# Optimization experiments

Measured on AMD Instinct MI355X. Metric: run time of the kernel, lower is better.

## Reference

```python
import jax, jax.numpy as jnp
import numpy as np

DIM = 512
HEADS = 16
WIN = 8  # window size (square)
B, H, W = 8, 128, 128
N = WIN * WIN  # tokens per window


def _relative_position_index(wh, ww):
    coords = np.stack(np.meshgrid(np.arange(wh), np.arange(ww), indexing='ij'))  # [2,wh,ww]
    cf = coords.reshape(2, -1)
    rel = cf[:, :, None] - cf[:, None, :]  # [2,n,n]
    rel = rel.transpose(1, 2, 0).astype(np.int32)
    rel[:, :, 0] += wh - 1
    rel[:, :, 1] += ww - 1
    rel[:, :, 0] *= 2 * ww - 1
    return rel.sum(-1)  # [n,n]


def setup_inputs() -> dict:
    key = jax.random.key(0)
    ks = jax.random.split(key, 8)
    std = 0.02
    return {
        'xa': jax.random.normal(ks[0], (B, DIM, H, W), jnp.float32),
        'xb': jax.random.normal(ks[1], (B, DIM, H, W), jnp.float32),
        'Wq': jax.random.normal(ks[2], (DIM, DIM), jnp.float32) * std,
        'bq': jnp.zeros((DIM,), jnp.float32),
        'Wkv': jax.random.normal(ks[3], (2 * DIM, DIM), jnp.float32) * std,
        'bkv': jnp.zeros((2 * DIM,), jnp.float32),
        'Wo': jax.random.normal(ks[4], (DIM, DIM), jnp.float32) * std,
        'bo': jnp.zeros((DIM,), jnp.float32),
        'rpb_table': jax.random.normal(ks[5], ((2 * WIN - 1) ** 2, HEADS), jnp.float32) * 0.01,
        'rel_idx': jnp.asarray(_relative_position_index(WIN, WIN)),
    }


def _windows(x):
    # [B,C,H,W] -> [B*r1*r2, N, C]
    b, c, h, w = x.shape
    r1, r2 = h // WIN, w // WIN
    x = x.reshape(b, c, r1, WIN, r2, WIN).transpose(0, 2, 4, 3, 5, 1)
    return x.reshape(b * r1 * r2, N, c)


def reference(xa, xb, Wq, bq, Wkv, bkv, Wo, bo, rpb_table, rel_idx):
    b, c, h, w = xa.shape
    r1, r2 = h // WIN, w // WIN
    head_dim = c // HEADS
    scale = head_dim ** -0.5

    qa = _windows(xa)  # [BM, N, C]
    kb = _windows(xb)

    q = jnp.einsum('bnc,oc->bno', qa, Wq) + bq
    kv = jnp.einsum('bnc,oc->bno', kb, Wkv) + bkv
    k, v = jnp.split(kv, 2, axis=2)
    q = q * scale

    def heads(t):  # [BM,N,C] -> [BM,H,N,hd]
        return t.reshape(t.shape[0], N, HEADS, head_dim).transpose(0, 2, 1, 3)

    q, k, v = heads(q), heads(k), heads(v)

    attn = jnp.einsum('bhmc,bhnc->bhmn', q, k)
    bias = rpb_table[rel_idx.reshape(-1)].reshape(N, N, HEADS).transpose(2, 0, 1)
    attn = attn + bias[None]
    attn = jax.nn.softmax(attn, axis=-1)

    out = jnp.einsum('bhmn,bhnc->bhmc', attn, v)
    out = out.transpose(0, 2, 1, 3).reshape(-1, N, c)
    out = jnp.einsum('bnc,oc->bno', out, Wo) + bo

    # [B*r1*r2, N, C] -> [B, C, H, W]
    out = out.reshape(b, r1, r2, WIN, WIN, c).transpose(0, 5, 1, 3, 2, 4)
    return out.reshape(b, c, h, w)
```

## Files before the change

kernel.cpp:

```cpp
#include <hip/hip_runtime.h>
#include <hip/hip_bf16.h>
#include <cstdint>
#include <cstddef>

typedef __attribute__((ext_vector_type(4))) float f32x4;
typedef __attribute__((ext_vector_type(8))) __bf16 bf16x8;
typedef __attribute__((ext_vector_type(8))) unsigned short ushort8;

__device__ __forceinline__ unsigned short f2b(float f) {
  unsigned int u = __float_as_uint(f);
  u = (u + 0x7fffu + ((u >> 16) & 1u)) >> 16;
  return (unsigned short)u;
}
__device__ __forceinline__ float b2f(unsigned short u) {
  return __uint_as_float(((unsigned int)u) << 16);
}

__device__ __forceinline__ f32x4 mfma_bf16(bf16x8 a, bf16x8 b, f32x4 c) {
  return __builtin_amdgcn_mfma_f32_16x16x32_bf16(a, b, c, 0, 0, 0);
}


__global__ void cvtw(const float* __restrict__ s, unsigned short* __restrict__ d, int n) {
  int i = blockIdx.x * 256 + threadIdx.x;
  if (i < n) d[i] = f2b(s[i]);
}

__global__ void bias_pre(const float* __restrict__ rpb, const int* __restrict__ rel,
                         float* __restrict__ biasf) {
  int i = blockIdx.x * 256 + threadIdx.x;
  int h = i >> 12, mn = i & 4095;
  biasf[i] = rpb[rel[mn] * 16 + h];
}

__global__ __launch_bounds__(256) void win_tr(const float* __restrict__ src,
                                              unsigned short* __restrict__ dst) {
  __shared__ float T[64 * 65];
  int bx = blockIdx.x;
  int win = bx >> 3, cg = bx & 7;
  int b = win >> 8, r1 = (win >> 4) & 15, r2 = win & 15;
  int h0 = r1 * 8, w0c = r2 * 8, c0 = cg * 64;
  int t = threadIdx.x;
#pragma unroll
  for (int pp = 0; pp < 2; ++pp) {
    int p = t + pp * 256;
    int cl = p >> 3, dy = p & 7;
    const float* sp = src + (((size_t)(b * 512 + c0 + cl) * 128 + (h0 + dy)) * 128 + w0c);
    float4 v0 = *(const float4*)sp;
    float4 v1 = *(const float4*)(sp + 4);
    int rb = dy * 8;
    T[(rb + 0) * 65 + cl] = v0.x; T[(rb + 1) * 65 + cl] = v0.y;
    T[(rb + 2) * 65 + cl] = v0.z; T[(rb + 3) * 65 + cl] = v0.w;
    T[(rb + 4) * 65 + cl] = v1.x; T[(rb + 5) * 65 + cl] = v1.y;
    T[(rb + 6) * 65 + cl] = v1.z; T[(rb + 7) * 65 + cl] = v1.w;
  }
  __syncthreads();
  int n = t >> 2, q = t & 3;
  union { unsigned short u[8]; int4 v; } pk0, pk1;
#pragma unroll
  for (int i = 0; i < 8; ++i) pk0.u[i] = f2b(T[n * 65 + q * 16 + i]);
#pragma unroll
  for (int i = 0; i < 8; ++i) pk1.u[i] = f2b(T[n * 65 + q * 16 + 8 + i]);
  size_t o = ((size_t)win * 64 + n) * 512 + c0 + q * 16;
  *(int4*)(dst + o) = pk0.v;
  *(int4*)(dst + o + 8) = pk1.v;
}

__global__ __launch_bounds__(256) void inv_tr(const unsigned short* __restrict__ Ot,
                                              float* __restrict__ out) {
  __shared__ float T[64 * 65];
  int bx = blockIdx.x;
  int win = bx >> 3, cg = bx & 7;
  int b = win >> 8, r1 = (win >> 4) & 15, r2 = win & 15;
  int h0 = r1 * 8, w0c = r2 * 8, c0 = cg * 64;
  int t = threadIdx.x;
  int n = t >> 2, q = t & 3;
  const unsigned short* sp = Ot + ((size_t)win * 64 + n) * 512 + c0 + q * 16;
  union { unsigned short u[8]; int4 v; } r0, r1u;
  r0.v = *(const int4*)sp;
  r1u.v = *(const int4*)(sp + 8);
#pragma unroll
  for (int i = 0; i < 8; ++i) {
    T[(q * 16 + i) * 65 + n] = b2f(r0.u[i]);
    T[(q * 16 + 8 + i) * 65 + n] = b2f(r1u.u[i]);
  }
  __syncthreads();
#pragma unroll
  for (int pp = 0; pp < 2; ++pp) {
    int p = t + pp * 256;
    int cl = p >> 3, dy = p & 7;
    int rb = dy * 8;
    float4 a, bv;
    a.x = T[cl * 65 + rb + 0]; a.y = T[cl * 65 + rb + 1];
    a.z = T[cl * 65 + rb + 2]; a.w = T[cl * 65 + rb + 3];
    bv.x = T[cl * 65 + rb + 4]; bv.y = T[cl * 65 + rb + 5];
    bv.z = T[cl * 65 + rb + 6]; bv.w = T[cl * 65 + rb + 7];
    float* dp = out + (((size_t)(b * 512 + c0 + cl) * 128 + (h0 + dy)) * 128 + w0c);
    *(float4*)dp = a;
    *(float4*)(dp + 4) = bv;
  }
}

template <int MODE, int NTL>
__global__ __launch_bounds__(256) void gemm_nt(const unsigned short* __restrict__ A,
                                               const unsigned short* __restrict__ W,
                                               const float* __restrict__ bias,
                                               unsigned short* __restrict__ out0,
                                               unsigned short* __restrict__ out1) {
  __shared__ __align__(16) unsigned short As[2][128 * 40];
  __shared__ __align__(16) unsigned short Bs[2][128 * 40];
  int bid = blockIdx.x;
  int cpx = gridDim.x >> 3;
  int wg = (bid & 7) * cpx + (bid >> 3);
  int tn = wg & ((1 << NTL) - 1);
  int tm = wg >> NTL;
  int m0 = tm * 128, n0 = tn * 128;
  int tid = threadIdx.x;
  int w = tid >> 6, lane = tid & 63, g = lane >> 4, c16 = lane & 15;
  int wr = w >> 1, wc = w & 1;
  int srow = tid >> 2, sq = tid & 3;
  const unsigned short* Ap0 = A + (size_t)(m0 + srow) * 512 + sq * 8;
  const unsigned short* Ap1 = Ap0 + 64 * 512;
  const unsigned short* Wp0 = W + (size_t)(n0 + srow) * 512 + sq * 8;
  const unsigned short* Wp1 = Wp0 + 64 * 512;
  int sA0 = srow * 40 + sq * 8;
  int sA1 = (srow + 64) * 40 + sq * 8;
  int aoff = (wr * 64 + c16) * 40 + g * 8;
  int boff = (wc * 64 + c16) * 40 + g * 8;

  int4 ra0 = *(const int4*)Ap0;
  int4 ra1 = *(const int4*)Ap1;
  int4 rb0 = *(const int4*)Wp0;
  int4 rb1 = *(const int4*)Wp1;
  *(int4*)&As[0][sA0] = ra0; *(int4*)&As[0][sA1] = ra1;
  *(int4*)&Bs[0][sA0] = rb0; *(int4*)&Bs[0][sA1] = rb1;
  __syncthreads();

  f32x4 z = {0.f, 0.f, 0.f, 0.f};
  f32x4 acc[4][4];
#pragma unroll
  for (int i = 0; i < 4; ++i)
#pragma unroll
    for (int j = 0; j < 4; ++j) acc[i][j] = z;

  for (int kt = 0; kt < 16; ++kt) {
    int cur = kt & 1;
    bf16x8 af[4], bfv[4];
#pragma unroll
    for (int i = 0; i < 4; ++i) {
      af[i]  = *(const bf16x8*)&As[cur][aoff + i * 640];
      bfv[i] = *(const bf16x8*)&Bs[cur][boff + i * 640];
    }
    if (kt < 15) {
      ra0 = *(const int4*)(Ap0 + (kt + 1) * 32);
      ra1 = *(const int4*)(Ap1 + (kt + 1) * 32);
      rb0 = *(const int4*)(Wp0 + (kt + 1) * 32);
      rb1 = *(const int4*)(Wp1 + (kt + 1) * 32);
    }
#pragma unroll
    for (int fm = 0; fm < 4; ++fm)
#pragma unroll
      for (int fn = 0; fn < 4; ++fn)
        acc[fm][fn] = mfma_bf16(af[fm], bfv[fn], acc[fm][fn]);
    if (kt < 15) {
      int nxt = cur ^ 1;
      *(int4*)&As[nxt][sA0] = ra0; *(int4*)&As[nxt][sA1] = ra1;
      *(int4*)&Bs[nxt][sA0] = rb0; *(int4*)&Bs[nxt][sA1] = rb1;
    }
    __syncthreads();
  }

  int mbase = m0 + wr * 64;
  int nbase = n0 + wc * 64;
#pragma unroll
  for (int fn = 0; fn < 4; ++fn) {
    int o = nbase + fn * 16 + c16;
    float bv = bias[o];
#pragma unroll
    for (int fm = 0; fm < 4; ++fm) {
      f32x4 v = acc[fm][fn];
#pragma unroll
      for (int r = 0; r < 4; ++r) {
        int tt = mbase + fm * 16 + g * 4 + r;
        float val = v[r] + bv;
        if constexpr (MODE == 0) {
          val *= 0.17677669529663688f;
          size_t idx = ((size_t)(tt >> 6) * 16 + (o >> 5)) * 2048 + (size_t)(tt & 63) * 32 + (o & 31);
          out0[idx] = f2b(val);
        } else if constexpr (MODE == 1) {
          int ol = o & 511;
          unsigned short* dst = (o < 512) ? out0 : out1;
          size_t idx = ((size_t)(tt >> 6) * 16 + (ol >> 5)) * 2048 + (size_t)(tt & 63) * 32 + (ol & 31);
          dst[idx] = f2b(val);
        } else {
          out0[(size_t)tt * 512 + o] = f2b(val);
        }
      }
    }
  }
}

#define SWZ(row, byte) ((byte) ^ (((((row) & 7) ^ (((row) >> 3) & 1))) << 4))

__global__ __launch_bounds__(256) void attn_win(const unsigned short* __restrict__ Qb,
                                                const unsigned short* __restrict__ Kb,
                                                const unsigned short* __restrict__ Vb,
                                                const float* __restrict__ biasf,
                                                unsigned short* __restrict__ Oattn) {
  __shared__ __align__(16) unsigned short Pl[4][4096];
  __shared__ __align__(16) unsigned short Vt[4][2048];
  int win = blockIdx.x;
  int tid = threadIdx.x, w = tid >> 6, lane = tid & 63;
  int g = lane >> 4, c16 = lane & 15;
  char* P  = (char*)Pl[w];
  char* VT = (char*)Vt[w];
  f32x4 z = {0.f, 0.f, 0.f, 0.f};
  for (int hh = 0; hh < 4; ++hh) {
    int h = w * 4 + hh;
    const bf16x8* qp = (const bf16x8*)(Qb + ((size_t)win * 16 + h) * 2048);
    const bf16x8* kp = (const bf16x8*)(Kb + ((size_t)win * 16 + h) * 2048);
    bf16x8 qf[4], kf[4];
#pragma unroll
    for (int i = 0; i < 4; ++i) {
      qf[i] = qp[(i * 16 + c16) * 4 + g];
      kf[i] = kp[(i * 16 + c16) * 4 + g];
    }
    f32x4 s[4][4];
#pragma unroll
    for (int i = 0; i < 4; ++i)
#pragma unroll
      for (int j = 0; j < 4; ++j) s[i][j] = z;
#pragma unroll
    for (int fm = 0; fm < 4; ++fm)
#pragma unroll
      for (int fn = 0; fn < 4; ++fn)
        s[fm][fn] = mfma_bf16(qf[fm], kf[fn], s[fm][fn]);

    const float* bh = biasf + h * 4096;
#pragma unroll
    for (int fm = 0; fm < 4; ++fm) {
#pragma unroll
      for (int r = 0; r < 4; ++r) {
        int m = fm * 16 + g * 4 + r;
        float vals[4];
#pragma unroll
        for (int fn = 0; fn < 4; ++fn)
          vals[fn] = s[fm][fn][r] + bh[m * 64 + fn * 16 + c16];
        float mx = fmaxf(fmaxf(vals[0], vals[1]), fmaxf(vals[2], vals[3]));
        mx = fmaxf(mx, __shfl_xor(mx, 1));
        mx = fmaxf(mx, __shfl_xor(mx, 2));
        mx = fmaxf(mx, __shfl_xor(mx, 4));
        mx = fmaxf(mx, __shfl_xor(mx, 8));
        float sum = 0.f;
#pragma unroll
        for (int fn = 0; fn < 4; ++fn) { vals[fn] = __expf(vals[fn] - mx); sum += vals[fn]; }
        sum += __shfl_xor(sum, 1);
        sum += __shfl_xor(sum, 2);
        sum += __shfl_xor(sum, 4);
        sum += __shfl_xor(sum, 8);
        float inv = 1.0f / sum;
#pragma unroll
        for (int fn = 0; fn < 4; ++fn) {
          int col = fn * 16 + c16;
          int byte = SWZ(m, m * 128 + col * 2);
          *(unsigned short*)(P + byte) = f2b(vals[fn] * inv);
        }
      }
    }
    const ushort8* vp = (const ushort8*)(Vb + ((size_t)win * 16 + h) * 2048);
#pragma unroll
    for (int i = 0; i < 4; ++i) {
      ushort8 vv = vp[(i * 16 + c16) * 4 + g];
#pragma unroll
      for (int j = 0; j < 8; ++j) {
        int row = g * 8 + j;
        int col = i * 16 + c16;
        int byte = SWZ(row, row * 128 + col * 2);
        *(unsigned short*)(VT + byte) = vv[j];
      }
    }
    f32x4 oa[4][2];
#pragma unroll
    for (int i = 0; i < 4; ++i) { oa[i][0] = z; oa[i][1] = z; }
#pragma unroll
    for (int ks = 0; ks < 2; ++ks) {
      bf16x8 pa[4], vbf[2];
#pragma unroll
      for (int fm = 0; fm < 4; ++fm) {
        int row = fm * 16 + c16;
        pa[fm] = *(const bf16x8*)(P + SWZ(row, row * 128 + ks * 64 + g * 16));
      }
#pragma unroll
      for (int fc = 0; fc < 2; ++fc) {
        int row = fc * 16 + c16;
        vbf[fc] = *(const bf16x8*)(VT + SWZ(row, row * 128 + ks * 64 + g * 16));
      }
#pragma unroll
      for (int fm = 0; fm < 4; ++fm)
#pragma unroll
        for (int fc = 0; fc < 2; ++fc)
          oa[fm][fc] = mfma_bf16(pa[fm], vbf[fc], oa[fm][fc]);
    }
#pragma unroll
    for (int fm = 0; fm < 4; ++fm)
#pragma unroll
      for (int fc = 0; fc < 2; ++fc)
#pragma unroll
        for (int r = 0; r < 4; ++r) {
          int m = fm * 16 + g * 4 + r;
          Oattn[((size_t)win * 64 + m) * 512 + h * 32 + fc * 16 + c16] = f2b(oa[fm][fc][r]);
        }
  }
}

extern "C" void kernel_launch(void* const* d_in, const int* in_sizes, int n_in,
                              void* d_out, int out_size, void* d_ws, size_t ws_size,
                              hipStream_t stream) {
  const float* xa  = (const float*)d_in[0];
  const float* xb  = (const float*)d_in[1];
  const float* Wq  = (const float*)d_in[2];
  const float* bq  = (const float*)d_in[3];
  const float* Wkv = (const float*)d_in[4];
  const float* bkv = (const float*)d_in[5];
  const float* Wo  = (const float*)d_in[6];
  const float* bo  = (const float*)d_in[7];
  const float* rpb = (const float*)d_in[8];
  const int*   rel = (const int*)d_in[9];
  float* out = (float*)d_out;

  char* ws = (char*)d_ws;
  unsigned short* R0 = (unsigned short*)ws;
  unsigned short* Qb = (unsigned short*)(ws + (size_t)134217728);
  unsigned short* Ot = Qb;
  unsigned short* Kb = (unsigned short*)d_out;
  unsigned short* Vb = Kb + (size_t)67108864;
  char* extra        = ws + (size_t)268435456;
  float* biasf          = (float*)extra;
  unsigned short* WqB   = (unsigned short*)(extra + 262144);
  unsigned short* WkvB  = (unsigned short*)(extra + 262144 + 524288);
  unsigned short* WoB   = (unsigned short*)(extra + 262144 + 524288 + 1048576);

  cvtw<<<1024, 256, 0, stream>>>(Wq,  WqB,  262144);
  cvtw<<<2048, 256, 0, stream>>>(Wkv, WkvB, 524288);
  cvtw<<<1024, 256, 0, stream>>>(Wo,  WoB,  262144);
  bias_pre<<<256, 256, 0, stream>>>(rpb, rel, biasf);

  win_tr<<<16384, 256, 0, stream>>>(xa, R0);
  gemm_nt<0, 2><<<4096, 256, 0, stream>>>(R0, WqB, bq, Qb, nullptr);
  win_tr<<<16384, 256, 0, stream>>>(xb, R0);
  gemm_nt<1, 3><<<8192, 256, 0, stream>>>(R0, WkvB, bkv, Kb, Vb);
  attn_win<<<2048, 256, 0, stream>>>(Qb, Kb, Vb, biasf, R0);
  gemm_nt<2, 2><<<4096, 256, 0, stream>>>(R0, WoB, bo, Ot, nullptr);
  inv_tr<<<16384, 256, 0, stream>>>(Ot, out);
}
```

Before: 1.461 ms.

## Load GEMM tiles directly into LDS and stream attention P per 16-row chunk

The bf16 GEMM now uses global_load_lds to copy A and W tiles straight from global memory into unpadded LDS buffers. This replaces the register round-trip and explicit LDS stores, and the next tile is issued at the top of each k-step. The attention kernel now writes softmax probabilities into a 16-row LDS scratch and runs the P·V MFMAs per row block, with V fragments preloaded once per head. LDS use and register pressure drop, but removing the padding may add LDS bank conflicts on fragment reads.

```diff
diff --git a/kernel.cpp b/kernel.cpp
--- a/kernel.cpp
+++ b/kernel.cpp
@@ -7,6 +7,9 @@
 typedef __attribute__((ext_vector_type(8))) __bf16 bf16x8;
 typedef __attribute__((ext_vector_type(8))) unsigned short ushort8;
 
+typedef __attribute__((address_space(3))) unsigned int lds_u32;
+typedef const __attribute__((address_space(1))) unsigned int glb_u32;
+
 __device__ __forceinline__ unsigned short f2b(float f) {
   unsigned int u = __float_as_uint(f);
   u = (u + 0x7fffu + ((u >> 16) & 1u)) >> 16;
@@ -18,6 +21,10 @@
 
 __device__ __forceinline__ f32x4 mfma_bf16(bf16x8 a, bf16x8 b, f32x4 c) {
   return __builtin_amdgcn_mfma_f32_16x16x32_bf16(a, b, c, 0, 0, 0);
+}
+
+__device__ __forceinline__ void gload16(const unsigned short* g, void* l) {
+  __builtin_amdgcn_global_load_lds((glb_u32*)g, (lds_u32*)l, 16, 0, 0);
 }
 
 
@@ -107,8 +114,8 @@
                                                const float* __restrict__ bias,
                                                unsigned short* __restrict__ out0,
                                                unsigned short* __restrict__ out1) {
-  __shared__ __align__(16) unsigned short As[2][128 * 40];
-  __shared__ __align__(16) unsigned short Bs[2][128 * 40];
+  __shared__ __align__(16) unsigned short As[2][128 * 32];
+  __shared__ __align__(16) unsigned short Bs[2][128 * 32];
   int bid = blockIdx.x;
   int cpx = gridDim.x >> 3;
   int wg = (bid & 7) * cpx + (bid >> 3);
@@ -118,22 +125,23 @@
   int tid = threadIdx.x;
   int w = tid >> 6, lane = tid & 63, g = lane >> 4, c16 = lane & 15;
   int wr = w >> 1, wc = w & 1;
-  int srow = tid >> 2, sq = tid & 3;
-  const unsigned short* Ap0 = A + (size_t)(m0 + srow) * 512 + sq * 8;
-  const unsigned short* Ap1 = Ap0 + 64 * 512;
-  const unsigned short* Wp0 = W + (size_t)(n0 + srow) * 512 + sq * 8;
-  const unsigned short* Wp1 = Wp0 + 64 * 512;
-  int sA0 = srow * 40 + sq * 8;
-  int sA1 = (srow + 64) * 40 + sq * 8;
-  int aoff = (wr * 64 + c16) * 40 + g * 8;
-  int boff = (wc * 64 + c16) * 40 + g * 8;
-
-  int4 ra0 = *(const int4*)Ap0;
-  int4 ra1 = *(const int4*)Ap1;
-  int4 rb0 = *(const int4*)Wp0;
-  int4 rb1 = *(const int4*)Wp1;
-  *(int4*)&As[0][sA0] = ra0; *(int4*)&As[0][sA1] = ra1;
-  *(int4*)&Bs[0][sA0] = rb0; *(int4*)&Bs[0][sA1] = rb1;
+
+  int r0 = tid >> 2, cc0 = (tid & 3) * 8;
+  int r1 = (256 + tid) >> 2, cc1 = (tid & 3) * 8;
+  const unsigned short* Ag0 = A + (size_t)(m0 + r0) * 512 + cc0;
+  const unsigned short* Ag1 = A + (size_t)(m0 + r1) * 512 + cc1;
+  const unsigned short* Wg0 = W + (size_t)(n0 + r0) * 512 + cc0;
+  const unsigned short* Wg1 = W + (size_t)(n0 + r1) * 512 + cc1;
+
+#define STAGE(b, kk) { \
+    char* la = (char*)As[b] + w * 1024; \
+    char* lb = (char*)Bs[b] + w * 1024; \
+    gload16(Ag0 + (kk) * 32, la); \
+    gload16(Ag1 + (kk) * 32, la + 4096); \
+    gload16(Wg0 + (kk) * 32, lb); \
+    gload16(Wg1 + (kk) * 32, lb + 4096); }
+
+  STAGE(0, 0);
   __syncthreads();
 
   f32x4 z = {0.f, 0.f, 0.f, 0.f};
@@ -143,32 +151,26 @@
 #pragma unroll
     for (int j = 0; j < 4; ++j) acc[i][j] = z;
 
+  int aoff = (wr * 64 + c16) * 64 + g * 16;
+  int boff = (wc * 64 + c16) * 64 + g * 16;
+
   for (int kt = 0; kt < 16; ++kt) {
     int cur = kt & 1;
+    if (kt < 15) STAGE(cur ^ 1, kt + 1);
     bf16x8 af[4], bfv[4];
 #pragma unroll
     for (int i = 0; i < 4; ++i) {
-      af[i]  = *(const bf16x8*)&As[cur][aoff + i * 640];
-      bfv[i] = *(const bf16x8*)&Bs[cur][boff + i * 640];
-    }
-    if (kt < 15) {
-      ra0 = *(const int4*)(Ap0 + (kt + 1) * 32);
-      ra1 = *(const int4*)(Ap1 + (kt + 1) * 32);
-      rb0 = *(const int4*)(Wp0 + (kt + 1) * 32);
-      rb1 = *(const int4*)(Wp1 + (kt + 1) * 32);
+      af[i]  = *(const bf16x8*)((char*)As[cur] + aoff + i * 1024);
+      bfv[i] = *(const bf16x8*)((char*)Bs[cur] + boff + i * 1024);
     }
 #pragma unroll
     for (int fm = 0; fm < 4; ++fm)
 #pragma unroll
       for (int fn = 0; fn < 4; ++fn)
         acc[fm][fn] = mfma_bf16(af[fm], bfv[fn], acc[fm][fn]);
-    if (kt < 15) {
-      int nxt = cur ^ 1;
-      *(int4*)&As[nxt][sA0] = ra0; *(int4*)&As[nxt][sA1] = ra1;
-      *(int4*)&Bs[nxt][sA0] = rb0; *(int4*)&Bs[nxt][sA1] = rb1;
-    }
     __syncthreads();
   }
+#undef STAGE
 
   int mbase = m0 + wr * 64;
   int nbase = n0 + wc * 64;
@@ -207,7 +209,7 @@
                                                 const unsigned short* __restrict__ Vb,
                                                 const float* __restrict__ biasf,
                                                 unsigned short* __restrict__ Oattn) {
-  __shared__ __align__(16) unsigned short Pl[4][4096];
+  __shared__ __align__(16) unsigned short Pl[4][1024];
   __shared__ __align__(16) unsigned short Vt[4][2048];
   int win = blockIdx.x;
   int tid = threadIdx.x, w = tid >> 6, lane = tid & 63;
@@ -236,12 +238,34 @@
       for (int fn = 0; fn < 4; ++fn)
         s[fm][fn] = mfma_bf16(qf[fm], kf[fn], s[fm][fn]);
 
+    const ushort8* vp = (const ushort8*)(Vb + ((size_t)win * 16 + h) * 2048);
+#pragma unroll
+    for (int i = 0; i < 4; ++i) {
+      ushort8 vv = vp[(i * 16 + c16) * 4 + g];
+#pragma unroll
+      for (int j = 0; j < 8; ++j) {
+        int row = g * 8 + j;
+        int col = i * 16 + c16;
+        int byte = SWZ(row, row * 128 + col * 2);
+        *(unsigned short*)(VT + byte) = vv[j];
+      }
+    }
+    bf16x8 vbf[2][2];
+#pragma unroll
+    for (int ks = 0; ks < 2; ++ks)
+#pragma unroll
+      for (int fc = 0; fc < 2; ++fc) {
+        int row = fc * 16 + c16;
+        vbf[ks][fc] = *(const bf16x8*)(VT + SWZ(row, row * 128 + ks * 64 + g * 16));
+      }
+
     const float* bh = biasf + h * 4096;
 #pragma unroll
     for (int fm = 0; fm < 4; ++fm) {
 #pragma unroll
       for (int r = 0; r < 4; ++r) {
         int m = fm * 16 + g * 4 + r;
+        int lm = g * 4 + r;
         float vals[4];
 #pragma unroll
         for (int fn = 0; fn < 4; ++fn)
@@ -262,54 +286,25 @@
 #pragma unroll
         for (int fn = 0; fn < 4; ++fn) {
           int col = fn * 16 + c16;
-          int byte = SWZ(m, m * 128 + col * 2);
+          int byte = SWZ(lm, lm * 128 + col * 2);
           *(unsigned short*)(P + byte) = f2b(vals[fn] * inv);
         }
       }
-    }
-    const ushort8* vp = (const ushort8*)(Vb + ((size_t)win * 16 + h) * 2048);
-#pragma unroll
-    for (int i = 0; i < 4; ++i) {
-      ushort8 vv = vp[(i * 16 + c16) * 4 + g];
-#pragma unroll
-      for (int j = 0; j < 8; ++j) {
-        int row = g * 8 + j;
-        int col = i * 16 + c16;
-        int byte = SWZ(row, row * 128 + col * 2);
-        *(unsigned short*)(VT + byte) = vv[j];
-      }
-    }
-    f32x4 oa[4][2];
-#pragma unroll
-    for (int i = 0; i < 4; ++i) { oa[i][0] = z; oa[i][1] = z; }
-#pragma unroll
-    for (int ks = 0; ks < 2; ++ks) {
-      bf16x8 pa[4], vbf[2];
-#pragma unroll
-      for (int fm = 0; fm < 4; ++fm) {
-        int row = fm * 16 + c16;
-        pa[fm] = *(const bf16x8*)(P + SWZ(row, row * 128 + ks * 64 + g * 16));
-      }
-#pragma unroll
-      for (int fc = 0; fc < 2; ++fc) {
-        int row = fc * 16 + c16;
-        vbf[fc] = *(const bf16x8*)(VT + SWZ(row, row * 128 + ks * 64 + g * 16));
-      }
-#pragma unroll
-      for (int fm = 0; fm < 4; ++fm)
-#pragma unroll
-        for (int fc = 0; fc < 2; ++fc)
-          oa[fm][fc] = mfma_bf16(pa[fm], vbf[fc], oa[fm][fc]);
-    }
-#pragma unroll
-    for (int fm = 0; fm < 4; ++fm)
-#pragma unroll
-      for (int fc = 0; fc < 2; ++fc)
-#pragma unroll
-        for (int r = 0; r < 4; ++r) {
-          int m = fm * 16 + g * 4 + r;
-          Oattn[((size_t)win * 64 + m) * 512 + h * 32 + fc * 16 + c16] = f2b(oa[fm][fc][r]);
-        }
+      bf16x8 pa0 = *(const bf16x8*)(P + SWZ(c16, c16 * 128 + g * 16));
+      bf16x8 pa1 = *(const bf16x8*)(P + SWZ(c16, c16 * 128 + 64 + g * 16));
+      f32x4 o0 = z, o1 = z;
+      o0 = mfma_bf16(pa0, vbf[0][0], o0);
+      o0 = mfma_bf16(pa1, vbf[1][0], o0);
+      o1 = mfma_bf16(pa0, vbf[0][1], o1);
+      o1 = mfma_bf16(pa1, vbf[1][1], o1);
+#pragma unroll
+      for (int r = 0; r < 4; ++r) {
+        int m = fm * 16 + g * 4 + r;
+        size_t ob = ((size_t)win * 64 + m) * 512 + h * 32;
+        Oattn[ob + c16] = f2b(o0[r]);
+        Oattn[ob + 16 + c16] = f2b(o1[r]);
+      }
+    }
   }
 }
 
```

After: 1.390 ms. 1.05x faster.
